# Performance work log

Measured on AMD Instinct MI355X. Metric: run time of the kernel, lower is better.

The kernel has to match this reference:

```python
import jax, jax.numpy as jnp
import numpy as np

H = 16       # query heads
KV = 4       # kv heads
BASE = 10000.0


def _rope(seq_len, head_dim, dtype):
    inv_freq = 1.0 / (BASE ** (jnp.arange(0, head_dim, 2, dtype=jnp.float32) / head_dim))
    t = jnp.arange(seq_len, dtype=jnp.float32)
    freqs = jnp.einsum('i,j->ij', t, inv_freq)          # [S, D/2]
    emb = jnp.concatenate([freqs, freqs], axis=-1)      # [S, D]
    return jnp.cos(emb).astype(dtype), jnp.sin(emb).astype(dtype)


def _rotate_half(x):
    x1, x2 = jnp.split(x, 2, axis=-1)
    return jnp.concatenate([-x2, x1], axis=-1)


def setup_inputs() -> dict:
    key = jax.random.key(0)
    ks = jax.random.split(key, 5)
    B, S, E = 2, 2048, 1024
    return {
        'x': jax.random.normal(ks[0], (B, S, E), jnp.float32),
        'wq': jax.random.normal(ks[1], (E, E), jnp.float32) * (E ** -0.5),
        'wk': jax.random.normal(ks[2], (KV * (E // H), E), jnp.float32) * (E ** -0.5),
        'wv': jax.random.normal(ks[3], (KV * (E // H), E), jnp.float32) * (E ** -0.5),
        'wo': jax.random.normal(ks[4], (E, E), jnp.float32) * (E ** -0.5),
    }


def reference(x, wq, wk, wv, wo):
    B, S, E = x.shape
    D = E // H
    G = H // KV  # query heads per kv head
    scale = D ** -0.5

    q = (x @ wq.T).reshape(B, S, H, D).transpose(0, 2, 1, 3)    # [B,H,S,D]
    k = (x @ wk.T).reshape(B, S, KV, D).transpose(0, 2, 1, 3)   # [B,KV,S,D]
    v = (x @ wv.T).reshape(B, S, KV, D).transpose(0, 2, 1, 3)   # [B,KV,S,D]

    cos, sin = _rope(S, D, x.dtype)                              # [S,D] each
    q = q * cos + _rotate_half(q) * sin
    k = k * cos + _rotate_half(k) * sin

    # GQA: group query heads per kv head instead of materializing repeated K/V
    qg = q.reshape(B, KV, G, S, D)
    scores = jnp.einsum('bkgsd,bktd->bkgst', qg, k) * scale      # [B,KV,G,S,S]
    causal = jnp.triu(jnp.ones((S, S), dtype=bool), k=1)
    scores = jnp.where(causal, jnp.finfo(scores.dtype).min, scores)
    attn = jax.nn.softmax(scores, axis=-1)
    out = jnp.einsum('bkgst,bktd->bkgsd', attn, v)               # [B,KV,G,S,D]
    out = out.reshape(B, H, S, D).transpose(0, 2, 1, 3).reshape(B, S, E)
    return out @ wo.T
```

## Files before the change

kernel.cpp:

```cpp
#include <hip/hip_runtime.h>
#include <stdint.h>

typedef unsigned short u16;
typedef __attribute__((ext_vector_type(8))) short s16x8;
typedef __attribute__((ext_vector_type(4))) float f32x4;
typedef __attribute__((ext_vector_type(4))) unsigned short u16x4;
typedef __attribute__((ext_vector_type(2))) unsigned int u32x2;


__device__ __forceinline__ u16 f2bf(float f) {
  unsigned u = __float_as_uint(f);
  unsigned r = (u + 0x7fffu + ((u >> 16) & 1u)) >> 16;
  return (u16)r;
}
__device__ __forceinline__ unsigned cvt_pk(float lo, float hi) {
  unsigned r;
  asm("v_cvt_pk_bf16_f32 %0, %1, %2" : "=v"(r) : "v"(lo), "v"(hi));
  return r;
}
__device__ __forceinline__ float exp2fast(float x) {
  return __builtin_amdgcn_exp2f(x);
}

typedef const __attribute__((address_space(1))) unsigned int* gas_ptr;
typedef __attribute__((address_space(3))) unsigned int* las_ptr;

__device__ __forceinline__ void g2l16(const void* g, void* l) {
  __builtin_amdgcn_global_load_lds((gas_ptr)g, (las_ptr)l, 16, 0, 0);
}

__device__ __forceinline__ void cvt4(const float* __restrict__ in, u16* __restrict__ out) {
  const f32x4 v = *(const f32x4*)in;
  u16x4 o;
  o[0] = f2bf(v[0]); o[1] = f2bf(v[1]); o[2] = f2bf(v[2]); o[3] = f2bf(v[3]);
  *(u16x4*)out = o;
}


__global__ void prep_kernel(const float* __restrict__ x,  const float* __restrict__ wq,
                            const float* __restrict__ wk, const float* __restrict__ wv,
                            const float* __restrict__ wo,
                            u16* __restrict__ xb, u16* __restrict__ wcat, u16* __restrict__ wob,
                            float* __restrict__ cosT, float* __restrict__ sinT) {
  const long id = (long)blockIdx.x * 256 + threadIdx.x;
  if (id < 262144) {
    cvt4(wq + id * 4, wcat + id * 4);
  } else if (id < 327680) {
    const long i = id - 262144;
    cvt4(wk + i * 4, wcat + 1048576 + i * 4);
  } else if (id < 393216) {
    const long i = id - 327680;
    cvt4(wv + i * 4, wcat + 1310720 + i * 4);
  } else if (id < 655360) {
    const long i = id - 393216;
    cvt4(wo + i * 4, wob + i * 4);
  } else if (id < 671744) {
    const long t = id - 655360;
#pragma unroll
    for (int u = 0; u < 4; ++u) {
      const long idx = t * 4 + u;
      const int s = (int)(idx >> 5), j = (int)(idx & 31);
      const double invd = exp(-(double)j * 0.2878231366242558);
      const float a = (float)s * (float)invd;
      cosT[idx] = cosf(a);
      sinT[idx] = sinf(a);
    }
  } else {
    const long i = id - 671744;
    cvt4(x + i * 4, xb + i * 4);
  }
}


__global__ __launch_bounds__(256, 2) void gemm_qkv_kernel(
    const u16* __restrict__ A, const u16* __restrict__ W,
    u16* __restrict__ qo, u16* __restrict__ ko, u16* __restrict__ vto,
    const float* __restrict__ cosT, const float* __restrict__ sinT) {
  const int K = 1024;
  __shared__ __align__(16) u16 As[2][128 * 64];
  __shared__ __align__(16) u16 Bs[2][128 * 64];
  const int tid = threadIdx.x;
  const int lane = tid & 63;
  const int wave = tid >> 6;
  const int g = lane >> 4, l15 = lane & 15;
  const int wr = wave >> 1, wc = wave & 1;
  const int bid = blockIdx.x;
  const int arowBlk = (bid & 7) * 4 + ((bid >> 3) & 3);
  const int wcolBlk = bid >> 5;
  const long arow0 = (long)arowBlk * 128;
  const long wrow0 = (long)wcolBlk * 128;
  const u16* Ab = A + arow0 * K;
  const u16* Wb = W + wrow0 * K;
  const bool isV = (wcolBlk >= 10);

  auto STAGE = [&](int buf, int k0) {
#pragma unroll
    for (int i = 0; i < 4; ++i) {
      const int lbase = i * 256 + wave * 64;
      const int c = lbase + lane;
      const int r = c >> 3, c8 = c & 7;
      const int cs = (c8 ^ (r & 7)) * 8;
      g2l16(Ab + (long)r * K + k0 + cs, (char*)As[buf] + lbase * 16);
      g2l16(Wb + (long)r * K + k0 + cs, (char*)Bs[buf] + lbase * 16);
    }
  };

  f32x4 acc[4][4] = {};
  int cur = 0;
  STAGE(0, 0);

  for (int k0 = 0; k0 < K; k0 += 64) {
    if (k0 + 64 < K) {
      STAGE(cur ^ 1, k0 + 64);
      asm volatile("s_waitcnt vmcnt(8)" ::: "memory");
    } else {
      asm volatile("s_waitcnt vmcnt(0)" ::: "memory");
    }
    __builtin_amdgcn_s_barrier();
#pragma unroll
    for (int ks = 0; ks < 2; ++ks) {
      s16x8 af[4], bfr[4];
#pragma unroll
      for (int m = 0; m < 4; ++m) {
        const int row = wr * 64 + m * 16 + l15;
        af[m] = *(const s16x8*)((const char*)As[cur] + row * 128 + (((ks * 4 + g) ^ (row & 7)) << 4));
      }
#pragma unroll
      for (int n = 0; n < 4; ++n) {
        const int row = wc * 64 + n * 16 + l15;
        bfr[n] = *(const s16x8*)((const char*)Bs[cur] + row * 128 + (((ks * 4 + g) ^ (row & 7)) << 4));
      }
      __builtin_amdgcn_s_setprio(1);
      if (!isV) {
#pragma unroll
        for (int m = 0; m < 4; ++m)
#pragma unroll
          for (int n = 0; n < 4; ++n)
            acc[m][n] = __builtin_amdgcn_mfma_f32_16x16x32_bf16(af[m], bfr[n], acc[m][n], 0, 0, 0);
      } else {
#pragma unroll
        for (int m = 0; m < 4; ++m)
#pragma unroll
          for (int n = 0; n < 4; ++n)
            acc[m][n] = __builtin_amdgcn_mfma_f32_16x16x32_bf16(bfr[m], af[n], acc[m][n], 0, 0, 0);
      }
      __builtin_amdgcn_s_setprio(0);
    }
    __builtin_amdgcn_s_barrier();
    cur ^= 1;
  }

  const int colBase = (int)wrow0 + wc * 64;
  const int j0 = l15;
  const float QSCALE = 0.18033688011112042f;

  if (colBase < 1024) {
    const int h2 = colBase >> 6;
#pragma unroll
    for (int m = 0; m < 4; ++m) {
      const int grow = (int)arow0 + wr * 64 + m * 16 + g * 4;
#pragma unroll
      for (int r = 0; r < 4; ++r) {
        const int row = grow + r;
        const int s = row & 2047, bb = row >> 11;
        const long ob = (((long)(bb * 16 + h2)) * 2048 + s) * 64;
        const float c0 = cosT[s * 32 + j0],      s0 = sinT[s * 32 + j0];
        const float c1 = cosT[s * 32 + 16 + j0], s1 = sinT[s * 32 + 16 + j0];
        qo[ob + j0]      = f2bf((acc[m][0][r] * c0 - acc[m][2][r] * s0) * QSCALE);
        qo[ob + 16 + j0] = f2bf((acc[m][1][r] * c1 - acc[m][3][r] * s1) * QSCALE);
        qo[ob + 32 + j0] = f2bf((acc[m][2][r] * c0 + acc[m][0][r] * s0) * QSCALE);
        qo[ob + 48 + j0] = f2bf((acc[m][3][r] * c1 + acc[m][1][r] * s1) * QSCALE);
      }
    }
  } else if (colBase < 1280) {
    const int kvh2 = (colBase - 1024) >> 6;
#pragma unroll
    for (int m = 0; m < 4; ++m) {
      const int grow = (int)arow0 + wr * 64 + m * 16 + g * 4;
#pragma unroll
      for (int r = 0; r < 4; ++r) {
        const int row = grow + r;
        const int s = row & 2047, bb = row >> 11;
        const long ob = (((long)(bb * 4 + kvh2)) * 2048 + s) * 64;
        const float c0 = cosT[s * 32 + j0],      s0 = sinT[s * 32 + j0];
        const float c1 = cosT[s * 32 + 16 + j0], s1 = sinT[s * 32 + 16 + j0];
        ko[ob + j0]      = f2bf(acc[m][0][r] * c0 - acc[m][2][r] * s0);
        ko[ob + 16 + j0] = f2bf(acc[m][1][r] * c1 - acc[m][3][r] * s1);
        ko[ob + 32 + j0] = f2bf(acc[m][2][r] * c0 + acc[m][0][r] * s0);
        ko[ob + 48 + j0] = f2bf(acc[m][3][r] * c1 + acc[m][1][r] * s1);
      }
    }
  } else {
    const int kvh2 = (colBase - 1280) >> 6;
    const int bb = (int)(arow0 >> 11);
    const int sBase = (int)(arow0 & 2047) + wr * 64;
    const long vrow0 = ((long)(bb * 4 + kvh2)) * 64;
#pragma unroll
    for (int mw = 0; mw < 4; ++mw) {
      const int d0 = mw * 16 + g * 4;
#pragma unroll
      for (int r = 0; r < 4; ++r) {
        const long db = (vrow0 + d0 + r) * 2048;
#pragma unroll
        for (int nx = 0; nx < 4; ++nx)
          vto[db + sBase + nx * 16 + l15] = f2bf(acc[mw][nx][r]);
      }
    }
  }
}


__global__ __launch_bounds__(256, 2) void gemm_out_kernel(
    const u16* __restrict__ A, const u16* __restrict__ W, float* __restrict__ Y) {
  const int K = 1024, N = 1024;
  __shared__ __align__(16) u16 As[2][128 * 64];
  __shared__ __align__(16) u16 Bs[2][128 * 64];
  const int tid = threadIdx.x;
  const int lane = tid & 63;
  const int wave = tid >> 6;
  const int g = lane >> 4, l15 = lane & 15;
  const int wr = wave >> 1, wc = wave & 1;
  const int bid = blockIdx.x;
  const int arowBlk = (bid & 7) * 4 + ((bid >> 3) & 3);
  const int wcolBlk = bid >> 5;
  const long arow0 = (long)arowBlk * 128;
  const long wrow0 = (long)wcolBlk * 128;
  const u16* Ab = A + arow0 * K;
  const u16* Wb = W + wrow0 * K;

  auto STAGE = [&](int buf, int k0) {
#pragma unroll
    for (int i = 0; i < 4; ++i) {
      const int lbase = i * 256 + wave * 64;
      const int c = lbase + lane;
      const int r = c >> 3, c8 = c & 7;
      const int cs = (c8 ^ (r & 7)) * 8;
      g2l16(Ab + (long)r * K + k0 + cs, (char*)As[buf] + lbase * 16);
      g2l16(Wb + (long)r * K + k0 + cs, (char*)Bs[buf] + lbase * 16);
    }
  };

  f32x4 acc[4][4] = {};
  int cur = 0;
  STAGE(0, 0);

  for (int k0 = 0; k0 < K; k0 += 64) {
    if (k0 + 64 < K) {
      STAGE(cur ^ 1, k0 + 64);
      asm volatile("s_waitcnt vmcnt(8)" ::: "memory");
    } else {
      asm volatile("s_waitcnt vmcnt(0)" ::: "memory");
    }
    __builtin_amdgcn_s_barrier();
#pragma unroll
    for (int ks = 0; ks < 2; ++ks) {
      s16x8 af[4], bfr[4];
#pragma unroll
      for (int m = 0; m < 4; ++m) {
        const int row = wr * 64 + m * 16 + l15;
        af[m] = *(const s16x8*)((const char*)As[cur] + row * 128 + (((ks * 4 + g) ^ (row & 7)) << 4));
      }
#pragma unroll
      for (int n = 0; n < 4; ++n) {
        const int row = wc * 64 + n * 16 + l15;
        bfr[n] = *(const s16x8*)((const char*)Bs[cur] + row * 128 + (((ks * 4 + g) ^ (row & 7)) << 4));
      }
      __builtin_amdgcn_s_setprio(1);
#pragma unroll
      for (int m = 0; m < 4; ++m)
#pragma unroll
        for (int n = 0; n < 4; ++n)
          acc[m][n] = __builtin_amdgcn_mfma_f32_16x16x32_bf16(af[m], bfr[n], acc[m][n], 0, 0, 0);
      __builtin_amdgcn_s_setprio(0);
    }
    __builtin_amdgcn_s_barrier();
    cur ^= 1;
  }

#pragma unroll
  for (int m = 0; m < 4; ++m)
#pragma unroll
    for (int n = 0; n < 4; ++n) {
      const long gr0 = arow0 + wr * 64 + m * 16 + g * 4;
      const long gc = wrow0 + wc * 64 + n * 16 + l15;
#pragma unroll
      for (int r = 0; r < 4; ++r)
        Y[(gr0 + r) * N + gc] = acc[m][n][r];
    }
}


__global__ __launch_bounds__(256, 2) void flash_kernel(
    const u16* __restrict__ qg,
    const u16* __restrict__ kg,
    const u16* __restrict__ vtg,
    u16* __restrict__ og) {
  const int tid = threadIdx.x, lane = tid & 63, w = tid >> 6;
  const int g = lane >> 4, l15 = lane & 15;

  const int bid = blockIdx.x;
  const int lid = (bid & 7) * 64 + (bid >> 3);
  const int pr = lid & 15, h = (lid >> 4) & 15, b = lid >> 8;
  const int kvh = h >> 2;

  __shared__ __align__(16) u16 Kl[3][64 * 64];
  __shared__ __align__(16) u16 Vl[3][64 * 64];
  __shared__ __align__(16) u16 Pl[4][16 * 64];

  const u16* Kp = kg  + ((long)(b * 4 + kvh)) * 2048 * 64;
  const u16* Vp = vtg + ((long)(b * 4 + kvh)) * 64 * 2048;

  auto STAGE = [&](int buf, int kt) {
#pragma unroll
    for (int j = 0; j < 2; ++j) {
      const int lbase = j * 256 + w * 64;
      const int c = lbase + lane;
      const int row = c >> 3, c8 = c & 7;
      const int cs = (c8 ^ (row & 7)) * 8;
      g2l16(Kp + ((long)(kt * 64 + row)) * 64 + cs, (char*)Kl[buf] + lbase * 16);
      g2l16(Vp + (long)row * 2048 + kt * 64 + cs,  (char*)Vl[buf] + lbase * 16);
    }
  };

#pragma unroll 1
  for (int pass = 0; pass < 2; ++pass) {
    const int qt = pass ? (31 - pr) : pr;
    const u16* Qp = qg + (((long)(b * 16 + h)) * 2048 + qt * 64 + w * 16) * 64;
    const s16x8 qf0 = *(const s16x8*)(Qp + l15 * 64 + g * 8);
    const s16x8 qf1 = *(const s16x8*)(Qp + l15 * 64 + 32 + g * 8);

    f32x4 of[4] = {};
    float m = -1e30f, lsum = 0.f;
    const int qrow = qt * 64 + w * 16 + l15;

    int cb = 0;
    STAGE(0, 0);

#pragma unroll 1
    for (int kt = 0; kt <= qt; ++kt) {
      const int nb = (cb == 2) ? 0 : cb + 1;
      if (kt < qt) {
        STAGE(nb, kt + 1);
        asm volatile("s_waitcnt vmcnt(4)" ::: "memory");
      } else {
        asm volatile("s_waitcnt vmcnt(0)" ::: "memory");
      }
      __builtin_amdgcn_s_barrier();
      const u16* Kb = Kl[cb];
      const u16* Vb = Vl[cb];

      f32x4 sf[4] = {};
      __builtin_amdgcn_s_setprio(1);
#pragma unroll
      for (int ks = 0; ks < 2; ++ks) {
        const s16x8 qv = ks ? qf1 : qf0;
#pragma unroll
        for (int fn = 0; fn < 4; ++fn) {
          const int row = fn * 16 + l15;
          const s16x8 kf = *(const s16x8*)((const char*)Kb + row * 128 + (((ks * 4 + g) ^ (row & 7)) << 4));
          sf[fn] = __builtin_amdgcn_mfma_f32_16x16x32_bf16(kf, qv, sf[fn], 0, 0, 0);
        }
      }
      __builtin_amdgcn_s_setprio(0);

      const bool diag = (kt == qt);
      float p[16];
#pragma unroll
      for (int fn = 0; fn < 4; ++fn)
#pragma unroll
        for (int r = 0; r < 4; ++r) {
          float sv = sf[fn][r];
          if (diag) {
            const int kv = kt * 64 + fn * 16 + 4 * g + r;
            if (kv > qrow) sv = -1e30f;
          }
          p[fn * 4 + r] = sv;
        }
      const float t0 = fmaxf(fmaxf(p[0], p[1]), p[2]);
      const float t1 = fmaxf(fmaxf(p[3], p[4]), p[5]);
      const float t2 = fmaxf(fmaxf(p[6], p[7]), p[8]);
      const float t3 = fmaxf(fmaxf(p[9], p[10]), p[11]);
      const float t4 = fmaxf(fmaxf(p[12], p[13]), p[14]);
      float mx = fmaxf(fmaxf(fmaxf(t0, t1), t2), fmaxf(fmaxf(t3, t4), p[15]));
      mx = fmaxf(mx, __shfl_xor(mx, 16));
      mx = fmaxf(mx, __shfl_xor(mx, 32));

      if (!__all(mx - m <= 11.0f)) {
        const float mn = fmaxf(m, mx);
        const float al = exp2fast(m - mn);
        m = mn;
        lsum *= al;
        float alq[4];
#pragma unroll
        for (int r = 0; r < 4; ++r) alq[r] = __shfl(al, 4 * g + r);
#pragma unroll
        for (int fd = 0; fd < 4; ++fd)
#pragma unroll
          for (int r = 0; r < 4; ++r) of[fd][r] *= alq[r];
      }

#pragma unroll
      for (int i = 0; i < 16; ++i) p[i] = exp2fast(p[i] - m);
      const float s0 = (p[0] + p[1]) + (p[2] + p[3]);
      const float s1 = (p[4] + p[5]) + (p[6] + p[7]);
      const float s2 = (p[8] + p[9]) + (p[10] + p[11]);
      const float s3 = (p[12] + p[13]) + (p[14] + p[15]);
      float rs = (s0 + s1) + (s2 + s3);
      rs += __shfl_xor(rs, 16);
      rs += __shfl_xor(rs, 32);
      lsum += rs;

      char* Pw = (char*)Pl[w] + l15 * 128;
#pragma unroll
      for (int fn = 0; fn < 4; ++fn) {
        const u32x2 v2 = {cvt_pk(p[fn * 4 + 0], p[fn * 4 + 1]),
                          cvt_pk(p[fn * 4 + 2], p[fn * 4 + 3])};
        *(u32x2*)(Pw + ((((2 * fn + (g >> 1)) ^ (l15 & 7))) << 4) + ((g & 1) * 8)) = v2;
      }

      __builtin_amdgcn_s_setprio(1);
#pragma unroll
      for (int ks = 0; ks < 2; ++ks) {
        const s16x8 pa = *(const s16x8*)(Pw + (((ks * 4 + g) ^ (l15 & 7)) << 4));
#pragma unroll
        for (int fd = 0; fd < 4; ++fd) {
          const int vrow = fd * 16 + l15;
          const s16x8 vf = *(const s16x8*)((const char*)Vb + vrow * 128 + (((ks * 4 + g) ^ (vrow & 7)) << 4));
          of[fd] = __builtin_amdgcn_mfma_f32_16x16x32_bf16(pa, vf, of[fd], 0, 0, 0);
        }
      }
      __builtin_amdgcn_s_setprio(0);

      cb = nb;
    }

    __syncthreads();

    float linv[4];
#pragma unroll
    for (int r = 0; r < 4; ++r) linv[r] = 1.0f / __shfl(lsum, 4 * g + r);
    const long orow0 = (long)b * 2048 + qt * 64 + w * 16 + 4 * g;
#pragma unroll
    for (int r = 0; r < 4; ++r) {
      const long gb = (orow0 + r) * 1024 + h * 64;
#pragma unroll
      for (int fd = 0; fd < 4; ++fd)
        og[gb + fd * 16 + l15] = f2bf(of[fd][r] * linv[r]);
    }
  }
}


extern "C" void kernel_launch(void* const* d_in, const int* in_sizes, int n_in,
                              void* d_out, int out_size, void* d_ws, size_t ws_size,
                              hipStream_t stream) {
  (void)in_sizes; (void)n_in; (void)out_size; (void)ws_size;
  const float* x  = (const float*)d_in[0];
  const float* wq = (const float*)d_in[1];
  const float* wk = (const float*)d_in[2];
  const float* wv = (const float*)d_in[3];
  const float* wo = (const float*)d_in[4];
  float* out = (float*)d_out;

  char* p = (char*)d_ws;
  auto alloc = [&](size_t bytes) { char* r = p; p += (bytes + 255) & ~(size_t)255; return r; };

  u16* xb    = (u16*)alloc(4096ull * 1024 * 2);
  u16* wcat  = (u16*)alloc(1536ull * 1024 * 2);
  u16* wob   = (u16*)alloc(1024ull * 1024 * 2);
  u16* qrb   = (u16*)alloc(4096ull * 1024 * 2);
  u16* krb   = (u16*)alloc(4096ull * 256 * 2);
  u16* vtb   = (u16*)alloc(4096ull * 256 * 2);
  u16* aob   = (u16*)alloc(4096ull * 1024 * 2);
  float* cosT = (float*)alloc(2048ull * 32 * 4);
  float* sinT = (float*)alloc(2048ull * 32 * 4);

  prep_kernel<<<6720, 256, 0, stream>>>(x, wq, wk, wv, wo, xb, wcat, wob, cosT, sinT);

  gemm_qkv_kernel<<<384, 256, 0, stream>>>(xb, wcat, qrb, krb, vtb, cosT, sinT);

  flash_kernel<<<512, 256, 0, stream>>>(qrb, krb, vtb, aob);

  gemm_out_kernel<<<256, 256, 0, stream>>>(aob, wob, out);
}
```

Measured before the change: 166.9 us.

## Shrink GEMM tiles to 128x64 and software-pipeline PV MFMA in flash kernel

Both projection GEMMs switch from 128x128 to 128x64 tiles, which doubles the grid, raises the occupancy hint to three blocks, and changes block-to-tile mapping, so the work spreads over more CUs. The flash kernel moves to a 4-deep K/V ring and double-buffers P, so the P·V MFMAs of the previous tile are issued right after the current QK^T MFMAs, overlapping them with the softmax. The trade-off is more LDS per flash block and less operand reuse per GEMM tile.

```diff
diff --git a/kernel.cpp b/kernel.cpp
--- a/kernel.cpp
+++ b/kernel.cpp
@@ -72,26 +72,25 @@
 }
 
 
-__global__ __launch_bounds__(256, 2) void gemm_qkv_kernel(
+__global__ __launch_bounds__(256, 3) void gemm_qkv_kernel(
     const u16* __restrict__ A, const u16* __restrict__ W,
     u16* __restrict__ qo, u16* __restrict__ ko, u16* __restrict__ vto,
     const float* __restrict__ cosT, const float* __restrict__ sinT) {
   const int K = 1024;
   __shared__ __align__(16) u16 As[2][128 * 64];
-  __shared__ __align__(16) u16 Bs[2][128 * 64];
+  __shared__ __align__(16) u16 Bs[2][64 * 64];
   const int tid = threadIdx.x;
   const int lane = tid & 63;
   const int wave = tid >> 6;
   const int g = lane >> 4, l15 = lane & 15;
-  const int wr = wave >> 1, wc = wave & 1;
   const int bid = blockIdx.x;
-  const int arowBlk = (bid & 7) * 4 + ((bid >> 3) & 3);
+  const int arowBlk = bid & 31;
   const int wcolBlk = bid >> 5;
   const long arow0 = (long)arowBlk * 128;
-  const long wrow0 = (long)wcolBlk * 128;
+  const long wrow0 = (long)wcolBlk * 64;
   const u16* Ab = A + arow0 * K;
   const u16* Wb = W + wrow0 * K;
-  const bool isV = (wcolBlk >= 10);
+  const bool isV = (wcolBlk >= 20);
 
   auto STAGE = [&](int buf, int k0) {
 #pragma unroll
@@ -101,48 +100,55 @@
       const int r = c >> 3, c8 = c & 7;
       const int cs = (c8 ^ (r & 7)) * 8;
       g2l16(Ab + (long)r * K + k0 + cs, (char*)As[buf] + lbase * 16);
+    }
+#pragma unroll
+    for (int i = 0; i < 2; ++i) {
+      const int lbase = i * 256 + wave * 64;
+      const int c = lbase + lane;
+      const int r = c >> 3, c8 = c & 7;
+      const int cs = (c8 ^ (r & 7)) * 8;
       g2l16(Wb + (long)r * K + k0 + cs, (char*)Bs[buf] + lbase * 16);
     }
   };
 
-  f32x4 acc[4][4] = {};
+  f32x4 acc[8] = {};
   int cur = 0;
   STAGE(0, 0);
 
   for (int k0 = 0; k0 < K; k0 += 64) {
     if (k0 + 64 < K) {
       STAGE(cur ^ 1, k0 + 64);
-      asm volatile("s_waitcnt vmcnt(8)" ::: "memory");
+      asm volatile("s_waitcnt vmcnt(6)" ::: "memory");
     } else {
       asm volatile("s_waitcnt vmcnt(0)" ::: "memory");
     }
     __builtin_amdgcn_s_barrier();
 #pragma unroll
     for (int ks = 0; ks < 2; ++ks) {
-      s16x8 af[4], bfr[4];
-#pragma unroll
-      for (int m = 0; m < 4; ++m) {
-        const int row = wr * 64 + m * 16 + l15;
+      s16x8 af[2], bfr[4];
+#pragma unroll
+      for (int m = 0; m < 2; ++m) {
+        const int row = wave * 32 + m * 16 + l15;
         af[m] = *(const s16x8*)((const char*)As[cur] + row * 128 + (((ks * 4 + g) ^ (row & 7)) << 4));
       }
 #pragma unroll
       for (int n = 0; n < 4; ++n) {
-        const int row = wc * 64 + n * 16 + l15;
+        const int row = n * 16 + l15;
         bfr[n] = *(const s16x8*)((const char*)Bs[cur] + row * 128 + (((ks * 4 + g) ^ (row & 7)) << 4));
       }
       __builtin_amdgcn_s_setprio(1);
       if (!isV) {
 #pragma unroll
-        for (int m = 0; m < 4; ++m)
+        for (int m = 0; m < 2; ++m)
 #pragma unroll
           for (int n = 0; n < 4; ++n)
-            acc[m][n] = __builtin_amdgcn_mfma_f32_16x16x32_bf16(af[m], bfr[n], acc[m][n], 0, 0, 0);
+            acc[m * 4 + n] = __builtin_amdgcn_mfma_f32_16x16x32_bf16(af[m], bfr[n], acc[m * 4 + n], 0, 0, 0);
       } else {
 #pragma unroll
-        for (int m = 0; m < 4; ++m)
-#pragma unroll
-          for (int n = 0; n < 4; ++n)
-            acc[m][n] = __builtin_amdgcn_mfma_f32_16x16x32_bf16(bfr[m], af[n], acc[m][n], 0, 0, 0);
+        for (int nw = 0; nw < 4; ++nw)
+#pragma unroll
+          for (int mx = 0; mx < 2; ++mx)
+            acc[nw * 2 + mx] = __builtin_amdgcn_mfma_f32_16x16x32_bf16(bfr[nw], af[mx], acc[nw * 2 + mx], 0, 0, 0);
       }
       __builtin_amdgcn_s_setprio(0);
     }
@@ -150,15 +156,15 @@
     cur ^= 1;
   }
 
-  const int colBase = (int)wrow0 + wc * 64;
+  const int colBase = (int)wrow0;
   const int j0 = l15;
   const float QSCALE = 0.18033688011112042f;
 
   if (colBase < 1024) {
     const int h2 = colBase >> 6;
 #pragma unroll
-    for (int m = 0; m < 4; ++m) {
-      const int grow = (int)arow0 + wr * 64 + m * 16 + g * 4;
+    for (int m = 0; m < 2; ++m) {
+      const int grow = (int)arow0 + wave * 32 + m * 16 + g * 4;
 #pragma unroll
       for (int r = 0; r < 4; ++r) {
         const int row = grow + r;
@@ -166,17 +172,17 @@
         const long ob = (((long)(bb * 16 + h2)) * 2048 + s) * 64;
         const float c0 = cosT[s * 32 + j0],      s0 = sinT[s * 32 + j0];
         const float c1 = cosT[s * 32 + 16 + j0], s1 = sinT[s * 32 + 16 + j0];
-        qo[ob + j0]      = f2bf((acc[m][0][r] * c0 - acc[m][2][r] * s0) * QSCALE);
-        qo[ob + 16 + j0] = f2bf((acc[m][1][r] * c1 - acc[m][3][r] * s1) * QSCALE);
-        qo[ob + 32 + j0] = f2bf((acc[m][2][r] * c0 + acc[m][0][r] * s0) * QSCALE);
-        qo[ob + 48 + j0] = f2bf((acc[m][3][r] * c1 + acc[m][1][r] * s1) * QSCALE);
+        qo[ob + j0]      = f2bf((acc[m * 4 + 0][r] * c0 - acc[m * 4 + 2][r] * s0) * QSCALE);
+        qo[ob + 16 + j0] = f2bf((acc[m * 4 + 1][r] * c1 - acc[m * 4 + 3][r] * s1) * QSCALE);
+        qo[ob + 32 + j0] = f2bf((acc[m * 4 + 2][r] * c0 + acc[m * 4 + 0][r] * s0) * QSCALE);
+        qo[ob + 48 + j0] = f2bf((acc[m * 4 + 3][r] * c1 + acc[m * 4 + 1][r] * s1) * QSCALE);
       }
     }
   } else if (colBase < 1280) {
     const int kvh2 = (colBase - 1024) >> 6;
 #pragma unroll
-    for (int m = 0; m < 4; ++m) {
-      const int grow = (int)arow0 + wr * 64 + m * 16 + g * 4;
+    for (int m = 0; m < 2; ++m) {
+      const int grow = (int)arow0 + wave * 32 + m * 16 + g * 4;
 #pragma unroll
       for (int r = 0; r < 4; ++r) {
         const int row = grow + r;
@@ -184,26 +190,26 @@
         const long ob = (((long)(bb * 4 + kvh2)) * 2048 + s) * 64;
         const float c0 = cosT[s * 32 + j0],      s0 = sinT[s * 32 + j0];
         const float c1 = cosT[s * 32 + 16 + j0], s1 = sinT[s * 32 + 16 + j0];
-        ko[ob + j0]      = f2bf(acc[m][0][r] * c0 - acc[m][2][r] * s0);
-        ko[ob + 16 + j0] = f2bf(acc[m][1][r] * c1 - acc[m][3][r] * s1);
-        ko[ob + 32 + j0] = f2bf(acc[m][2][r] * c0 + acc[m][0][r] * s0);
-        ko[ob + 48 + j0] = f2bf(acc[m][3][r] * c1 + acc[m][1][r] * s1);
+        ko[ob + j0]      = f2bf(acc[m * 4 + 0][r] * c0 - acc[m * 4 + 2][r] * s0);
+        ko[ob + 16 + j0] = f2bf(acc[m * 4 + 1][r] * c1 - acc[m * 4 + 3][r] * s1);
+        ko[ob + 32 + j0] = f2bf(acc[m * 4 + 2][r] * c0 + acc[m * 4 + 0][r] * s0);
+        ko[ob + 48 + j0] = f2bf(acc[m * 4 + 3][r] * c1 + acc[m * 4 + 1][r] * s1);
       }
     }
   } else {
     const int kvh2 = (colBase - 1280) >> 6;
     const int bb = (int)(arow0 >> 11);
-    const int sBase = (int)(arow0 & 2047) + wr * 64;
+    const int sBase = ((int)arow0 & 2047) + wave * 32;
     const long vrow0 = ((long)(bb * 4 + kvh2)) * 64;
 #pragma unroll
-    for (int mw = 0; mw < 4; ++mw) {
-      const int d0 = mw * 16 + g * 4;
+    for (int nw = 0; nw < 4; ++nw) {
 #pragma unroll
       for (int r = 0; r < 4; ++r) {
-        const long db = (vrow0 + d0 + r) * 2048;
-#pragma unroll
-        for (int nx = 0; nx < 4; ++nx)
-          vto[db + sBase + nx * 16 + l15] = f2bf(acc[mw][nx][r]);
+        const int d = nw * 16 + 4 * g + r;
+        const long db = (vrow0 + d) * 2048 + sBase;
+#pragma unroll
+        for (int mx = 0; mx < 2; ++mx)
+          vto[db + mx * 16 + l15] = f2bf(acc[nw * 2 + mx][r]);
       }
     }
   }
@@ -214,17 +220,16 @@
     const u16* __restrict__ A, const u16* __restrict__ W, float* __restrict__ Y) {
   const int K = 1024, N = 1024;
   __shared__ __align__(16) u16 As[2][128 * 64];
-  __shared__ __align__(16) u16 Bs[2][128 * 64];
+  __shared__ __align__(16) u16 Bs[2][64 * 64];
   const int tid = threadIdx.x;
   const int lane = tid & 63;
   const int wave = tid >> 6;
   const int g = lane >> 4, l15 = lane & 15;
-  const int wr = wave >> 1, wc = wave & 1;
   const int bid = blockIdx.x;
-  const int arowBlk = (bid & 7) * 4 + ((bid >> 3) & 3);
+  const int arowBlk = bid & 31;
   const int wcolBlk = bid >> 5;
   const long arow0 = (long)arowBlk * 128;
-  const long wrow0 = (long)wcolBlk * 128;
+  const long wrow0 = (long)wcolBlk * 64;
   const u16* Ab = A + arow0 * K;
   const u16* Wb = W + wrow0 * K;
 
@@ -236,41 +241,48 @@
       const int r = c >> 3, c8 = c & 7;
       const int cs = (c8 ^ (r & 7)) * 8;
       g2l16(Ab + (long)r * K + k0 + cs, (char*)As[buf] + lbase * 16);
+    }
+#pragma unroll
+    for (int i = 0; i < 2; ++i) {
+      const int lbase = i * 256 + wave * 64;
+      const int c = lbase + lane;
+      const int r = c >> 3, c8 = c & 7;
+      const int cs = (c8 ^ (r & 7)) * 8;
       g2l16(Wb + (long)r * K + k0 + cs, (char*)Bs[buf] + lbase * 16);
     }
   };
 
-  f32x4 acc[4][4] = {};
+  f32x4 acc[8] = {};
   int cur = 0;
   STAGE(0, 0);
 
   for (int k0 = 0; k0 < K; k0 += 64) {
     if (k0 + 64 < K) {
       STAGE(cur ^ 1, k0 + 64);
-      asm volatile("s_waitcnt vmcnt(8)" ::: "memory");
+      asm volatile("s_waitcnt vmcnt(6)" ::: "memory");
     } else {
       asm volatile("s_waitcnt vmcnt(0)" ::: "memory");
     }
     __builtin_amdgcn_s_barrier();
 #pragma unroll
     for (int ks = 0; ks < 2; ++ks) {
-      s16x8 af[4], bfr[4];
-#pragma unroll
-      for (int m = 0; m < 4; ++m) {
-        const int row = wr * 64 + m * 16 + l15;
+      s16x8 af[2], bfr[4];
+#pragma unroll
+      for (int m = 0; m < 2; ++m) {
+        const int row = wave * 32 + m * 16 + l15;
         af[m] = *(const s16x8*)((const char*)As[cur] + row * 128 + (((ks * 4 + g) ^ (row & 7)) << 4));
       }
 #pragma unroll
       for (int n = 0; n < 4; ++n) {
-        const int row = wc * 64 + n * 16 + l15;
+        const int row = n * 16 + l15;
         bfr[n] = *(const s16x8*)((const char*)Bs[cur] + row * 128 + (((ks * 4 + g) ^ (row & 7)) << 4));
       }
       __builtin_amdgcn_s_setprio(1);
 #pragma unroll
-      for (int m = 0; m < 4; ++m)
+      for (int m = 0; m < 2; ++m)
 #pragma unroll
         for (int n = 0; n < 4; ++n)
-          acc[m][n] = __builtin_amdgcn_mfma_f32_16x16x32_bf16(af[m], bfr[n], acc[m][n], 0, 0, 0);
+          acc[m * 4 + n] = __builtin_amdgcn_mfma_f32_16x16x32_bf16(af[m], bfr[n], acc[m * 4 + n], 0, 0, 0);
       __builtin_amdgcn_s_setprio(0);
     }
     __builtin_amdgcn_s_barrier();
@@ -278,14 +290,14 @@
   }
 
 #pragma unroll
-  for (int m = 0; m < 4; ++m)
+  for (int m = 0; m < 2; ++m)
 #pragma unroll
     for (int n = 0; n < 4; ++n) {
-      const long gr0 = arow0 + wr * 64 + m * 16 + g * 4;
-      const long gc = wrow0 + wc * 64 + n * 16 + l15;
+      const long gr0 = arow0 + wave * 32 + m * 16 + g * 4;
+      const long gc = wrow0 + n * 16 + l15;
 #pragma unroll
       for (int r = 0; r < 4; ++r)
-        Y[(gr0 + r) * N + gc] = acc[m][n][r];
+        Y[(gr0 + r) * N + gc] = acc[m * 4 + n][r];
     }
 }
 
@@ -303,9 +315,9 @@
   const int pr = lid & 15, h = (lid >> 4) & 15, b = lid >> 8;
   const int kvh = h >> 2;
 
-  __shared__ __align__(16) u16 Kl[3][64 * 64];
-  __shared__ __align__(16) u16 Vl[3][64 * 64];
-  __shared__ __align__(16) u16 Pl[4][16 * 64];
+  __shared__ __align__(16) u16 Kl[4][64 * 64];
+  __shared__ __align__(16) u16 Vl[4][64 * 64];
+  __shared__ __align__(16) u16 Pl[4][2][16 * 64];
 
   const u16* Kp = kg  + ((long)(b * 4 + kvh)) * 2048 * 64;
   const u16* Vp = vtg + ((long)(b * 4 + kvh)) * 64 * 2048;
@@ -333,21 +345,18 @@
     float m = -1e30f, lsum = 0.f;
     const int qrow = qt * 64 + w * 16 + l15;
 
-    int cb = 0;
     STAGE(0, 0);
 
 #pragma unroll 1
     for (int kt = 0; kt <= qt; ++kt) {
-      const int nb = (cb == 2) ? 0 : cb + 1;
       if (kt < qt) {
-        STAGE(nb, kt + 1);
+        STAGE((kt + 1) & 3, kt + 1);
         asm volatile("s_waitcnt vmcnt(4)" ::: "memory");
       } else {
         asm volatile("s_waitcnt vmcnt(0)" ::: "memory");
       }
       __builtin_amdgcn_s_barrier();
-      const u16* Kb = Kl[cb];
-      const u16* Vb = Vl[cb];
+      const u16* Kb = Kl[kt & 3];
 
       f32x4 sf[4] = {};
       __builtin_amdgcn_s_setprio(1);
@@ -359,6 +368,21 @@
           const int row = fn * 16 + l15;
           const s16x8 kf = *(const s16x8*)((const char*)Kb + row * 128 + (((ks * 4 + g) ^ (row & 7)) << 4));
           sf[fn] = __builtin_amdgcn_mfma_f32_16x16x32_bf16(kf, qv, sf[fn], 0, 0, 0);
+        }
+      }
+
+      if (kt) {
+        const u16* Vbp = Vl[(kt - 1) & 3];
+        const char* Pr = (const char*)Pl[w][(kt - 1) & 1] + l15 * 128;
+#pragma unroll
+        for (int ks = 0; ks < 2; ++ks) {
+          const s16x8 pa = *(const s16x8*)(Pr + (((ks * 4 + g) ^ (l15 & 7)) << 4));
+#pragma unroll
+          for (int fd = 0; fd < 4; ++fd) {
+            const int vrow = fd * 16 + l15;
+            const s16x8 vf = *(const s16x8*)((const char*)Vbp + vrow * 128 + (((ks * 4 + g) ^ (vrow & 7)) << 4));
+            of[fd] = __builtin_amdgcn_mfma_f32_16x16x32_bf16(pa, vf, of[fd], 0, 0, 0);
+          }
         }
       }
       __builtin_amdgcn_s_setprio(0);
@@ -410,28 +434,30 @@
       rs += __shfl_xor(rs, 32);
       lsum += rs;
 
-      char* Pw = (char*)Pl[w] + l15 * 128;
+      char* Pw = (char*)Pl[w][kt & 1] + l15 * 128;
 #pragma unroll
       for (int fn = 0; fn < 4; ++fn) {
         const u32x2 v2 = {cvt_pk(p[fn * 4 + 0], p[fn * 4 + 1]),
                           cvt_pk(p[fn * 4 + 2], p[fn * 4 + 3])};
         *(u32x2*)(Pw + ((((2 * fn + (g >> 1)) ^ (l15 & 7))) << 4) + ((g & 1) * 8)) = v2;
       }
-
+    }
+
+    {
+      const u16* Vbp = Vl[qt & 3];
+      const char* Pr = (const char*)Pl[w][qt & 1] + l15 * 128;
       __builtin_amdgcn_s_setprio(1);
 #pragma unroll
       for (int ks = 0; ks < 2; ++ks) {
-        const s16x8 pa = *(const s16x8*)(Pw + (((ks * 4 + g) ^ (l15 & 7)) << 4));
+        const s16x8 pa = *(const s16x8*)(Pr + (((ks * 4 + g) ^ (l15 & 7)) << 4));
 #pragma unroll
         for (int fd = 0; fd < 4; ++fd) {
           const int vrow = fd * 16 + l15;
-          const s16x8 vf = *(const s16x8*)((const char*)Vb + vrow * 128 + (((ks * 4 + g) ^ (vrow & 7)) << 4));
+          const s16x8 vf = *(const s16x8*)((const char*)Vbp + vrow * 128 + (((ks * 4 + g) ^ (vrow & 7)) << 4));
           of[fd] = __builtin_amdgcn_mfma_f32_16x16x32_bf16(pa, vf, of[fd], 0, 0, 0);
         }
       }
       __builtin_amdgcn_s_setprio(0);
-
-      cb = nb;
     }
 
     __syncthreads();
@@ -477,9 +503,9 @@
 
   prep_kernel<<<6720, 256, 0, stream>>>(x, wq, wk, wv, wo, xb, wcat, wob, cosT, sinT);
 
-  gemm_qkv_kernel<<<384, 256, 0, stream>>>(xb, wcat, qrb, krb, vtb, cosT, sinT);
+  gemm_qkv_kernel<<<768, 256, 0, stream>>>(xb, wcat, qrb, krb, vtb, cosT, sinT);
 
   flash_kernel<<<512, 256, 0, stream>>>(qrb, krb, vtb, aob);
 
-  gemm_out_kernel<<<256, 256, 0, stream>>>(aob, wob, out);
-}
+  gemm_out_kernel<<<512, 256, 0, stream>>>(aob, wob, out);
+}
```

Result: faster. 162.2 us (-2.8%).
